# Optimization experiments

Hardware: AMD Instinct MI355X
Metric: run time of the kernel (lower is better)

Reference implementation:

```python
import jax, jax.numpy as jnp
import numpy as np

N_EDGES = 1_600_000
D_FEAT = 128
DIM_SIZE = 50_000


def setup_inputs() -> dict:
    key = jax.random.key(0)
    k1, k2, k3, k4 = jax.random.split(key, 4)
    src = jax.random.normal(k1, (N_EDGES, D_FEAT), dtype=jnp.float32)
    index = jax.random.randint(k2, (N_EDGES,), 0, DIM_SIZE, dtype=jnp.int32)
    # torch Linear(in=2*D, out=D): weight [D, 2*D] stored here transposed-friendly as [D, 2D]
    W = jax.random.normal(k3, (D_FEAT, 2 * D_FEAT), dtype=jnp.float32) / np.sqrt(2 * D_FEAT)
    b = jax.random.normal(k4, (D_FEAT,), dtype=jnp.float32) * 0.01
    return {"src": src, "index": index, "W": W, "b": b, "dim_size": DIM_SIZE}


def reference(src, index, W, b, dim_size):
    # scatter-add and scatter-max over segments, then concat on feature dim
    s_add = jax.ops.segment_sum(src, index, num_segments=dim_size)          # [dim_size, D]
    s_max = jax.ops.segment_max(src, index, num_segments=dim_size)          # [dim_size, D]
    # torch_scatter fills empty segments with 0 for max; jax uses -inf
    s_max = jnp.where(jnp.isneginf(s_max), jnp.zeros_like(s_max), s_max)
    out = jnp.concatenate([s_add, s_max], axis=-1)                          # [dim_size, 2D]
    # keep_same_dim linear projection: y = out @ W^T + b
    return jnp.einsum('nk,dk->nd', out, W) + b
```

## Files before the change

### kernel.cpp

```cpp
#include <hip/hip_runtime.h>
#include <math.h>

#define D_FEAT 128
#define SCAN_ITEMS 2048
#define NHB 256
#define HTHREADS 1024
#define MAXPAIR 25600

typedef float f32x4 __attribute__((ext_vector_type(4)));
typedef short short8 __attribute__((ext_vector_type(8)));

__device__ __forceinline__ unsigned short f2bf(float f) {
    unsigned int u = __float_as_uint(f);
    u += 0x7FFFu + ((u >> 16) & 1u);
    return (unsigned short)(u >> 16);
}

__global__ __launch_bounds__(HTHREADS) void hist_kernel(const int* __restrict__ index,
                                                        unsigned int* __restrict__ bhist,
                                                        const float* __restrict__ W,
                                                        unsigned short* __restrict__ Wfrag,
                                                        int* __restrict__ off,
                                                        int M, int npair, int n4, int n) {
    __shared__ unsigned int h[MAXPAIR];
    const int b = blockIdx.x, t = threadIdx.x;

    if (b == NHB - 1) {
        for (int i = t; i < 2 * D_FEAT * D_FEAT; i += HTHREADS) {
            int ii = i & 7, lf = (i >> 3) & 63, sf = (i >> 9) & 7, cf = i >> 12;
            int col = cf * 16 + (lf & 15);
            int k   = sf * 32 + ((lf >> 4) << 3) + ii;
            Wfrag[i] = f2bf(W[(size_t)col * (2 * D_FEAT) + k]);
        }
        if (t == 0) off[M] = n;
    }

    for (int j = t; j < npair; j += HTHREADS) h[j] = 0u;
    __syncthreads();

    const int per = (n4 + NHB - 1) / NHB;
    const int i0 = b * per;
    const int i1 = min(n4, i0 + per);
    const int4* idx4 = reinterpret_cast<const int4*>(index);
    for (int i = i0 + t; i < i1; i += HTHREADS) {
        int4 v = idx4[i];
        atomicAdd(&h[v.x >> 1], 1u << ((v.x & 1) << 4));
        atomicAdd(&h[v.y >> 1], 1u << ((v.y & 1) << 4));
        atomicAdd(&h[v.z >> 1], 1u << ((v.z & 1) << 4));
        atomicAdd(&h[v.w >> 1], 1u << ((v.w & 1) << 4));
    }
    if (b == 0) {
        for (int r = 4 * n4 + t; r < n; r += HTHREADS) {
            int v = index[r];
            atomicAdd(&h[v >> 1], 1u << ((v & 1) << 4));
        }
    }
    __syncthreads();

    unsigned int* dst = bhist + (size_t)b * npair;
    for (int j = t; j < npair; j += HTHREADS) dst[j] = h[j];
}

__global__ __launch_bounds__(256) void sumhist_kernel(const unsigned int* __restrict__ bhist,
                                                      int* __restrict__ cnt,
                                                      int npair, int M) {
    int i = blockIdx.x * 256 + threadIdx.x;
    if (i >= npair) return;
    int lo = 0, hi = 0;
    for (int b = 0; b < NHB; ++b) {
        unsigned int v = bhist[(size_t)b * npair + i];
        lo += (int)(v & 0xFFFFu);
        hi += (int)(v >> 16);
    }
    if (2 * i < M)     cnt[2 * i]     = lo;
    if (2 * i + 1 < M) cnt[2 * i + 1] = hi;
}

__global__ __launch_bounds__(256) void scan_kernel(const int* __restrict__ cnt,
                                                   int* __restrict__ off,
                                                   int* __restrict__ cursor, int n) {
    __shared__ int sh[SCAN_ITEMS];
    __shared__ int ts[256];
    __shared__ int pre[256];
    const int b = blockIdx.x, t = threadIdx.x;
    const int base = b * SCAN_ITEMS;

    int p = 0;
    for (int i = t; i < base; i += 256) p += cnt[i];
    pre[t] = p;
    __syncthreads();
    for (int st = 128; st > 0; st >>= 1) {
        if (t < st) pre[t] += pre[t + st];
        __syncthreads();
    }
    const int block_base = pre[0];
    __syncthreads();

    #pragma unroll
    for (int j = 0; j < 8; ++j) {
        int i = base + j * 256 + t;
        sh[j * 256 + t] = (i < n) ? cnt[i] : 0;
    }
    __syncthreads();
    int s = 0;
    #pragma unroll
    for (int j = 0; j < 8; ++j) s += sh[t * 8 + j];
    ts[t] = s;
    __syncthreads();
    for (int st = 1; st < 256; st <<= 1) {
        int u = (t >= st) ? ts[t - st] : 0;
        __syncthreads();
        ts[t] += u;
        __syncthreads();
    }
    int run = block_base + ts[t] - s;
    #pragma unroll
    for (int j = 0; j < 8; ++j) {
        int i = base + t * 8 + j;
        if (i < n) {
            off[i] = run;
            cursor[i] = run;
            run += sh[t * 8 + j];
        }
    }
}

__global__ __launch_bounds__(256) void order_kernel(const int* __restrict__ index,
                                                    int* __restrict__ cursor,
                                                    int* __restrict__ order, int n4, int n) {
    int i = blockIdx.x * 256 + threadIdx.x;
    if (i < n4) {
        int4 v = reinterpret_cast<const int4*>(index)[i];
        int e = 4 * i;
        order[atomicAdd(&cursor[v.x], 1)] = e;
        order[atomicAdd(&cursor[v.y], 1)] = e + 1;
        order[atomicAdd(&cursor[v.z], 1)] = e + 2;
        order[atomicAdd(&cursor[v.w], 1)] = e + 3;
    }
    int rem = 4 * n4 + i;
    if (i < n - 4 * n4) order[atomicAdd(&cursor[index[rem]], 1)] = rem;
}

__global__ __launch_bounds__(256) void redgemm_kernel(
    const float* __restrict__ src, const int* __restrict__ order,
    const int* __restrict__ off, const unsigned short* __restrict__ Wfrag,
    const float* __restrict__ bias, float* __restrict__ out, int M)
{
    __shared__ __align__(16) unsigned short atile[16][264];

    const int w    = threadIdx.x >> 6;
    const int lane = threadIdx.x & 63;
    const int half = lane >> 5;
    const int fl   = (lane & 31) << 2;
    const int seg0 = blockIdx.x * 16;

    for (int q = 0; q < 4; ++q) {
        const int seg = seg0 + w * 4 + q;
        const int r   = w * 4 + q;
        if (seg < M) {
            const int start = off[seg], end = off[seg + 1];

            f32x4 s0 = {0.f,0.f,0.f,0.f}, s1 = {0.f,0.f,0.f,0.f};
            f32x4 m0 = {-INFINITY,-INFINITY,-INFINITY,-INFINITY}, m1 = m0;

            for (int base = start; base < end; base += 64) {
                int idx = base + lane;
                int eo  = (idx < end) ? order[idx] : 0;
                int lim = end - base; if (lim > 64) lim = 64;
                for (int j = 0; j < lim; j += 4) {
                    int jj0 = j + half;
                    int jj1 = j + 2 + half;
                    int e0 = __shfl(eo, jj0);
                    int e1 = __shfl(eo, jj1);
                    if (jj0 < lim) {
                        f32x4 v = *reinterpret_cast<const f32x4*>(src + (size_t)e0 * D_FEAT + fl);
                        s0.x += v.x; s0.y += v.y; s0.z += v.z; s0.w += v.w;
                        m0.x = fmaxf(m0.x, v.x); m0.y = fmaxf(m0.y, v.y);
                        m0.z = fmaxf(m0.z, v.z); m0.w = fmaxf(m0.w, v.w);
                    }
                    if (jj1 < lim) {
                        f32x4 v = *reinterpret_cast<const f32x4*>(src + (size_t)e1 * D_FEAT + fl);
                        s1.x += v.x; s1.y += v.y; s1.z += v.z; s1.w += v.w;
                        m1.x = fmaxf(m1.x, v.x); m1.y = fmaxf(m1.y, v.y);
                        m1.z = fmaxf(m1.z, v.z); m1.w = fmaxf(m1.w, v.w);
                    }
                }
            }

            f32x4 s = {s0.x + s1.x, s0.y + s1.y, s0.z + s1.z, s0.w + s1.w};
            f32x4 m = {fmaxf(m0.x, m1.x), fmaxf(m0.y, m1.y),
                       fmaxf(m0.z, m1.z), fmaxf(m0.w, m1.w)};

            s.x += __shfl_xor(s.x, 32); s.y += __shfl_xor(s.y, 32);
            s.z += __shfl_xor(s.z, 32); s.w += __shfl_xor(s.w, 32);
            m.x = fmaxf(m.x, __shfl_xor(m.x, 32)); m.y = fmaxf(m.y, __shfl_xor(m.y, 32));
            m.z = fmaxf(m.z, __shfl_xor(m.z, 32)); m.w = fmaxf(m.w, __shfl_xor(m.w, 32));

            if (end == start) { m.x = 0.f; m.y = 0.f; m.z = 0.f; m.w = 0.f; }

            const f32x4 o = (half == 0) ? s : m;
            unsigned int lo = (unsigned int)f2bf(o.x) | ((unsigned int)f2bf(o.y) << 16);
            unsigned int hi = (unsigned int)f2bf(o.z) | ((unsigned int)f2bf(o.w) << 16);
            *reinterpret_cast<uint2*>(&atile[r][fl + half * D_FEAT]) = make_uint2(lo, hi);
        } else {
            *reinterpret_cast<uint2*>(&atile[r][fl + half * D_FEAT]) = make_uint2(0u, 0u);
        }
    }
    __syncthreads();

    f32x4 acc0 = {0.f,0.f,0.f,0.f}, acc1 = {0.f,0.f,0.f,0.f};
    const int arow = lane & 15;
    const int kgrp = (lane >> 4) << 3;
    #pragma unroll
    for (int s = 0; s < 8; ++s) {
        short8 a = *reinterpret_cast<const short8*>(&atile[arow][s * 32 + kgrp]);
        short8 b0 = *reinterpret_cast<const short8*>(Wfrag + (((size_t)((2*w  ) * 8 + s)) * 64 + lane) * 8);
        short8 b1 = *reinterpret_cast<const short8*>(Wfrag + (((size_t)((2*w+1) * 8 + s)) * 64 + lane) * 8);
        acc0 = __builtin_amdgcn_mfma_f32_16x16x32_bf16(a, b0, acc0, 0, 0, 0);
        acc1 = __builtin_amdgcn_mfma_f32_16x16x32_bf16(a, b1, acc1, 0, 0, 0);
    }

    const int r0   = (lane >> 4) << 2;
    const int colb = lane & 15;
    #pragma unroll
    for (int cc = 0; cc < 2; ++cc) {
        const f32x4 acc = cc ? acc1 : acc0;
        int col = (2 * w + cc) * 16 + colb;
        float bv = bias[col];
        #pragma unroll
        for (int r = 0; r < 4; ++r) {
            int row = seg0 + r0 + r;
            if (row < M) out[(size_t)row * D_FEAT + col] = acc[r] + bv;
        }
    }
}

extern "C" void kernel_launch(void* const* d_in, const int* in_sizes, int n_in,
                              void* d_out, int out_size, void* d_ws, size_t ws_size,
                              hipStream_t stream) {
    const float* src   = (const float*)d_in[0];
    const int*   index = (const int*)d_in[1];
    const float* W     = (const float*)d_in[2];
    const float* bias  = (const float*)d_in[3];

    const int n_edges = in_sizes[1];
    const int M       = out_size / D_FEAT;
    const int npair   = (M + 1) >> 1;

    unsigned short* Wfrag = (unsigned short*)d_ws;
    int*   cnt    = (int*)(Wfrag + 2 * D_FEAT * D_FEAT);
    int*   off    = cnt + M;
    int*   cursor = off + M + 1;
    int*   order  = cursor + M;
    unsigned int* bhist = (unsigned int*)(order + n_edges);

    const int nblk = (M + SCAN_ITEMS - 1) / SCAN_ITEMS;

    int n4 = n_edges / 4;
    hist_kernel<<<NHB, HTHREADS, 0, stream>>>(index, bhist, W, Wfrag, off,
                                              M, npair, n4, n_edges);
    sumhist_kernel<<<(npair + 255) / 256, 256, 0, stream>>>(bhist, cnt, npair, M);

    scan_kernel<<<nblk, 256, 0, stream>>>(cnt, off, cursor, M);

    int eb4 = (max(n4, n_edges - 4 * n4) + 255) / 256;
    order_kernel<<<eb4, 256, 0, stream>>>(index, cursor, order, n4, n_edges);

    redgemm_kernel<<<(M + 15) / 16, 256, 0, stream>>>(src, order, off, Wfrag, bias,
                                                      (float*)d_out, M);
}
```

Before: 367.4 us.

## Replace global-atomic scatter with per-block histogram prefix ranks in LDS

sumhist now rewrites each per-block histogram entry as an exclusive prefix across blocks. order_kernel loads its block's prefix row into shared memory and takes each edge's rank from packed 16-bit LDS atomics instead of global atomicAdd on a cursor array. This removes 1.6M contended global atomics and the cursor buffer, at the cost of one extra pass over bhist. Correctness relies on order_kernel's edge partitioning matching hist_kernel's, and on per-bucket counts fitting in 16 bits.

```diff
diff --git a/kernel.cpp b/kernel.cpp
--- a/kernel.cpp
+++ b/kernel.cpp
@@ -61,14 +61,16 @@
     for (int j = t; j < npair; j += HTHREADS) dst[j] = h[j];
 }
 
-__global__ __launch_bounds__(256) void sumhist_kernel(const unsigned int* __restrict__ bhist,
+__global__ __launch_bounds__(256) void sumhist_kernel(unsigned int* __restrict__ bhist,
                                                       int* __restrict__ cnt,
                                                       int npair, int M) {
     int i = blockIdx.x * 256 + threadIdx.x;
     if (i >= npair) return;
     int lo = 0, hi = 0;
     for (int b = 0; b < NHB; ++b) {
-        unsigned int v = bhist[(size_t)b * npair + i];
+        unsigned int* p = bhist + (size_t)b * npair + i;
+        unsigned int v = *p;
+        *p = (unsigned int)(lo & 0xFFFF) | ((unsigned int)hi << 16);
         lo += (int)(v & 0xFFFFu);
         hi += (int)(v >> 16);
     }
@@ -77,8 +79,7 @@
 }
 
 __global__ __launch_bounds__(256) void scan_kernel(const int* __restrict__ cnt,
-                                                   int* __restrict__ off,
-                                                   int* __restrict__ cursor, int n) {
+                                                   int* __restrict__ off, int n) {
     __shared__ int sh[SCAN_ITEMS];
     __shared__ int ts[256];
     __shared__ int pre[256];
@@ -119,26 +120,48 @@
         int i = base + t * 8 + j;
         if (i < n) {
             off[i] = run;
-            cursor[i] = run;
             run += sh[t * 8 + j];
         }
     }
 }
 
-__global__ __launch_bounds__(256) void order_kernel(const int* __restrict__ index,
-                                                    int* __restrict__ cursor,
-                                                    int* __restrict__ order, int n4, int n) {
-    int i = blockIdx.x * 256 + threadIdx.x;
-    if (i < n4) {
-        int4 v = reinterpret_cast<const int4*>(index)[i];
+__global__ __launch_bounds__(HTHREADS) void order_kernel(const int* __restrict__ index,
+                                                         const unsigned int* __restrict__ bhist,
+                                                         const int* __restrict__ off,
+                                                         int* __restrict__ order,
+                                                         int npair, int n4, int n) {
+    __shared__ unsigned int hl[MAXPAIR];
+    const int b = blockIdx.x, t = threadIdx.x;
+
+    const unsigned int* srcrow = bhist + (size_t)b * npair;
+    for (int j = t; j < npair; j += HTHREADS) hl[j] = srcrow[j];
+    __syncthreads();
+
+    const int per = (n4 + NHB - 1) / NHB;
+    const int i0 = b * per;
+    const int i1 = min(n4, i0 + per);
+    const int4* idx4 = reinterpret_cast<const int4*>(index);
+    for (int i = i0 + t; i < i1; i += HTHREADS) {
+        int4 v = idx4[i];
         int e = 4 * i;
-        order[atomicAdd(&cursor[v.x], 1)] = e;
-        order[atomicAdd(&cursor[v.y], 1)] = e + 1;
-        order[atomicAdd(&cursor[v.z], 1)] = e + 2;
-        order[atomicAdd(&cursor[v.w], 1)] = e + 3;
-    }
-    int rem = 4 * n4 + i;
-    if (i < n - 4 * n4) order[atomicAdd(&cursor[index[rem]], 1)] = rem;
+        #pragma unroll
+        for (int q = 0; q < 4; ++q) {
+            int s = (q == 0) ? v.x : (q == 1) ? v.y : (q == 2) ? v.z : v.w;
+            unsigned int sh = (unsigned int)((s & 1) << 4);
+            unsigned int old = atomicAdd(&hl[s >> 1], 1u << sh);
+            int rank = (int)((old >> sh) & 0xFFFFu);
+            order[off[s] + rank] = e + q;
+        }
+    }
+    if (b == 0) {
+        for (int r = 4 * n4 + t; r < n; r += HTHREADS) {
+            int s = index[r];
+            unsigned int sh = (unsigned int)((s & 1) << 4);
+            unsigned int old = atomicAdd(&hl[s >> 1], 1u << sh);
+            int rank = (int)((old >> sh) & 0xFFFFu);
+            order[off[s] + rank] = r;
+        }
+    }
 }
 
 __global__ __launch_bounds__(256) void redgemm_kernel(
@@ -250,8 +273,7 @@
     unsigned short* Wfrag = (unsigned short*)d_ws;
     int*   cnt    = (int*)(Wfrag + 2 * D_FEAT * D_FEAT);
     int*   off    = cnt + M;
-    int*   cursor = off + M + 1;
-    int*   order  = cursor + M;
+    int*   order  = off + M + 1;
     unsigned int* bhist = (unsigned int*)(order + n_edges);
 
     const int nblk = (M + SCAN_ITEMS - 1) / SCAN_ITEMS;
@@ -261,10 +283,10 @@
                                               M, npair, n4, n_edges);
     sumhist_kernel<<<(npair + 255) / 256, 256, 0, stream>>>(bhist, cnt, npair, M);
 
-    scan_kernel<<<nblk, 256, 0, stream>>>(cnt, off, cursor, M);
-
-    int eb4 = (max(n4, n_edges - 4 * n4) + 255) / 256;
-    order_kernel<<<eb4, 256, 0, stream>>>(index, cursor, order, n4, n_edges);
+    scan_kernel<<<nblk, 256, 0, stream>>>(cnt, off, M);
+
+    order_kernel<<<NHB, HTHREADS, 0, stream>>>(index, bhist, off, order,
+                                               npair, n4, n_edges);
 
     redgemm_kernel<<<(M + 15) / 16, 256, 0, stream>>>(src, order, off, Wfrag, bias,
                                                       (float*)d_out, M);
```

Measured after the change: 296.0 us. 1.24x faster.
